# Kernel tuning notes

Measured on AMD Instinct MI355X. Metric: run time of the kernel, lower is better.

## Reference

```python
import jax, jax.numpy as jnp
import numpy as np


def conv1x1(x, W, b):
    # x: [B,C,H,W], W: [O,C] (1x1 conv kernel squeezed), b: [O]
    return jnp.einsum('bchw,oc->bohw', x, W) + b[None, :, None, None]


def setup_inputs() -> dict:
    key = jax.random.key(0)
    ks = jax.random.split(key, 16)
    B, C, H, W = 4, 2048, 32, 32
    HID = 256  # gate_strength_fc hidden width
    s = 1.0 / np.sqrt(C)
    x = jax.random.normal(ks[0], (B, C, H, W), dtype=jnp.float32)
    mask = jax.random.uniform(ks[1], (B, 1, H, W)) > 0.8
    use_entropy_gate = jax.random.randint(ks[2], (B,), 0, 2).astype(bool)
    return {
        'x': x,
        'Wq': jax.random.normal(ks[3], (C, C)) * s,
        'bq': jnp.zeros((C,), jnp.float32),
        'Wk': jax.random.normal(ks[4], (C, C)) * s,
        'bk': jnp.zeros((C,), jnp.float32),
        'Wv': jax.random.normal(ks[5], (C, C)) * s,
        'bv': jnp.zeros((C,), jnp.float32),
        'Wg': jax.random.normal(ks[6], (C, C)) * s,
        'bg': jnp.zeros((C,), jnp.float32),
        'W1': jax.random.normal(ks[7], (HID, C)) * s,
        'b1': jnp.zeros((HID,), jnp.float32),
        'W2': jax.random.normal(ks[8], (1, HID)) * (1.0 / np.sqrt(HID)),
        'b2': jnp.zeros((1,), jnp.float32),
        'mask': mask,
        'use_entropy_gate': use_entropy_gate,
    }


def reference(x, Wq, bq, Wk, bk, Wv, bv, Wg, bg, W1, b1, W2, b2, mask, use_entropy_gate):
    B, C, H, W = x.shape
    HW = H * W
    masked_x = x * mask.astype(x.dtype)
    # 1x1 conv projections, flattened over spatial dims
    q = conv1x1(masked_x, Wq, bq).reshape(B, C, HW).transpose(0, 2, 1)  # [B,HW,C]
    k = conv1x1(masked_x, Wk, bk).reshape(B, C, HW)                     # [B,C,HW]
    v = conv1x1(x, Wv, bv).reshape(B, C, HW)                            # [B,C,HW]
    # attention[b,n,m] = softmax_m(q[b,n,:] . k[b,:,m])
    attn = jax.nn.softmax(jnp.einsum('bnc,bcm->bnm', q, k), axis=-1)    # [B,HW,HW]
    # out = bmm(value, attention^T): out[b,c,m] = sum_n v[b,c,n] * attn[b,m,n]
    out = jnp.einsum('bcn,bmn->bcm', v, attn).reshape(B, C, H, W)
    # gate strength head: 2048 -> 256 -> 1, then sigmoid
    gate_strength = jax.nn.sigmoid(conv1x1(jax.nn.relu(conv1x1(x, W1, b1)), W2, b2))  # [B,1,H,W]
    gate = jax.nn.sigmoid(conv1x1(x, Wg, bg))                                          # [B,C,H,W]
    gated = out * gate * gate_strength
    # per-sample select: gated attention output where flag set, else passthrough x
    return jnp.where(use_entropy_gate[:, None, None, None], gated, x)
```

## Files before the change

kernel.cpp:

```cpp
#include <hip/hip_runtime.h>
#include <cstddef>
#include <cstdint>


typedef unsigned int u32;
typedef unsigned short u16;
typedef __attribute__((ext_vector_type(8))) short bf16x8;
typedef __attribute__((ext_vector_type(4))) float f32x4;

#define B_   4
#define C_   2048
#define HW_  1024
#define HID_ 256
#define KP   384
#define NQK  384
#define NVGH 1088

#define WAITVM(N) asm volatile("s_waitcnt vmcnt(" #N ")" ::: "memory")
__device__ __forceinline__ void barw() {
  asm volatile("" ::: "memory");
  __builtin_amdgcn_s_barrier();
  asm volatile("" ::: "memory");
}

__device__ __forceinline__ float sigmoidf_(float x) {
  return 1.0f / (1.0f + __expf(-x));
}
__device__ __forceinline__ u16 f2bf(float f) {
  u32 u = __float_as_uint(f);
  return (u16)((u + 0x7FFFu + ((u >> 16) & 1u)) >> 16);
}
__device__ __forceinline__ float bf2f(u16 h) {
  return __uint_as_float(((u32)h) << 16);
}
__device__ __forceinline__ void gld16(void* lds, const void* g) {
  __builtin_amdgcn_global_load_lds(
      (const __attribute__((address_space(1))) u32*)g,
      (__attribute__((address_space(3))) u32*)lds, 16, 0, 0);
}

__device__ __forceinline__ void stage128x32s(u16* lds, const u16* g, int ld, int tid) {
#pragma unroll
  for (int t = 0; t < 2; ++t) {
    int s = tid + t * 256;
    int row = s >> 2;
    int oct = ((s & 3) - (row >> 1)) & 3;
    gld16(lds + (size_t)s * 8, g + (size_t)row * ld + oct * 8);
  }
}
template <int NF>
__device__ __forceinline__ void read_frags_s(const u16* lds, int base, int ln, int kq,
                                             bf16x8* f) {
#pragma unroll
  for (int t = 0; t < NF; ++t) {
    int row = base + t * 16 + ln;
    int oct = (kq + (row >> 1)) & 3;
    f[t] = *(const bf16x8*)(lds + (size_t)row * 32 + oct * 8);
  }
}

__device__ __forceinline__ void stage_qk4(u16* L, const u16* Ah, const u16* Al,
                                          const u16* Bh, const u16* Bl, int k0, int tid) {
  stage128x32s(L,         Ah + k0, C_, tid);
  stage128x32s(L + 4096,  Al + k0, C_, tid);
  stage128x32s(L + 8192,  Bh + k0, C_, tid);
  stage128x32s(L + 12288, Bl + k0, C_, tid);
}
__device__ __forceinline__ void stage_ab2(u16* L, const u16* A, const u16* Bp, int k0,
                                          int lda, int ldb, int tid) {
  stage128x32s(L,        A + k0, lda, tid);
  stage128x32s(L + 4096, Bp + k0, ldb, tid);
}
__device__ __forceinline__ void comp_qk(const u16* L, int wm, int wn, int ln, int kq,
                                        f32x4 (&acc)[4][4]) {
  bf16x8 ah[4], al[4], bh[4], bl[4];
  read_frags_s<4>(L, wm, ln, kq, ah);
  read_frags_s<4>(L + 4096, wm, ln, kq, al);
  read_frags_s<4>(L + 8192, wn, ln, kq, bh);
  read_frags_s<4>(L + 12288, wn, ln, kq, bl);
#pragma unroll
  for (int i = 0; i < 4; ++i)
#pragma unroll
    for (int j = 0; j < 4; ++j) {
      acc[i][j] = __builtin_amdgcn_mfma_f32_16x16x32_bf16(ah[i], bh[j], acc[i][j], 0, 0, 0);
      acc[i][j] = __builtin_amdgcn_mfma_f32_16x16x32_bf16(ah[i], bl[j], acc[i][j], 0, 0, 0);
      acc[i][j] = __builtin_amdgcn_mfma_f32_16x16x32_bf16(al[i], bh[j], acc[i][j], 0, 0, 0);
    }
}
__device__ __forceinline__ void comp_ab(const u16* L, int wm, int wn, int ln, int kq,
                                        f32x4 (&acc)[4][4]) {
  bf16x8 af[4], bg_[4];
  read_frags_s<4>(L, wm, ln, kq, af);
  read_frags_s<4>(L + 4096, wn, ln, kq, bg_);
#pragma unroll
  for (int i = 0; i < 4; ++i)
#pragma unroll
    for (int j = 0; j < 4; ++j)
      acc[i][j] = __builtin_amdgcn_mfma_f32_16x16x32_bf16(af[i], bg_[j], acc[i][j], 0, 0, 0);
}

__global__ __launch_bounds__(256)
void scan_mask(const int* __restrict__ mask, int* __restrict__ idx,
               int* __restrict__ rnk, int* __restrict__ cnt)
{
  const int b = blockIdx.x;
  const int t = threadIdx.x;
  __shared__ int base;
  if (t == 0) base = 0;
  __syncthreads();
  int m0 = t * 4;
  int mv[4], local = 0;
#pragma unroll
  for (int i = 0; i < 4; ++i) { mv[i] = mask[b * HW_ + m0 + i] != 0; local += mv[i]; }
  int my = atomicAdd(&base, local);
#pragma unroll
  for (int i = 0; i < 4; ++i) {
    if (mv[i]) {
      int r = my++;
      if (r < KP) { idx[b * KP + r] = m0 + i; rnk[b * HW_ + m0 + i] = r; }
      else rnk[b * HW_ + m0 + i] = -1;
    } else {
      rnk[b * HW_ + m0 + i] = -1;
    }
  }
  __syncthreads();
  if (t == 0) cnt[b] = min(base, KP);
}

__global__ __launch_bounds__(256)
void transpose_fused(const float* __restrict__ x, u16* __restrict__ xhi,
                     u16* __restrict__ xkh, u16* __restrict__ xkl,
                     const int* __restrict__ rnk, const int* __restrict__ useg)
{
  const int b = blockIdx.z;
  if (!useg[b]) return;
  __shared__ float t[32][33];
  const int c0 = blockIdx.y * 32, j0 = blockIdx.x * 32;
  const int tid = threadIdx.x;
  const float* xb = x + ((size_t)b * C_ + c0) * (size_t)HW_ + j0;
  {
    int jj = tid & 31, cs = tid >> 5;
#pragma unroll
    for (int t4 = 0; t4 < 4; ++t4) {
      int c = cs * 4 + t4;
      t[c][jj] = xb[(size_t)c * HW_ + jj];
    }
  }
  __syncthreads();
  int j = tid >> 3, c4 = (tid & 7) * 4;
  float v0 = t[c4 + 0][j], v1 = t[c4 + 1][j], v2 = t[c4 + 2][j], v3 = t[c4 + 3][j];
  ushort4 hv;
  hv.x = f2bf(v0); hv.y = f2bf(v1); hv.z = f2bf(v2); hv.w = f2bf(v3);
  *(ushort4*)(xhi + ((size_t)b * HW_ + j0 + j) * (size_t)C_ + c0 + c4) = hv;
  int r = rnk[b * HW_ + j0 + j];
  if (r >= 0) {
    ushort4 lv;
    lv.x = f2bf(v0 - bf2f(hv.x)); lv.y = f2bf(v1 - bf2f(hv.y));
    lv.z = f2bf(v2 - bf2f(hv.z)); lv.w = f2bf(v3 - bf2f(hv.w));
    size_t o = ((size_t)b * KP + r) * (size_t)C_ + c0 + c4;
    *(ushort4*)(xkh + o) = hv;
    *(ushort4*)(xkl + o) = lv;
  }
}

__global__ __launch_bounds__(256)
void cast_all(const float* __restrict__ Wq, const float* __restrict__ Wk,
              const float* __restrict__ Wv, const float* __restrict__ Wg,
              const float* __restrict__ W1,
              u16* __restrict__ Wqkh, u16* __restrict__ Wqkl, u16* __restrict__ Wvgh)
{
  const int reg = blockIdx.y;
  int i = (blockIdx.x * 256 + threadIdx.x) * 4;
  const float* src; u16* dh; u16* dl = nullptr; int n = C_ * C_;
  if (reg == 0)      { src = Wq; dh = Wqkh;              dl = Wqkl; }
  else if (reg == 1) { src = Wk; dh = Wqkh + C_ * C_;    dl = Wqkl + C_ * C_; }
  else if (reg == 2) { src = Wv; dh = Wvgh; }
  else if (reg == 3) { src = Wg; dh = Wvgh + C_ * C_; }
  else               { src = W1; dh = Wvgh + 2 * C_ * C_; n = HID_ * C_; }
  if (i >= n) return;
  float4 v = *(const float4*)(src + i);
  ushort4 h;
  h.x = f2bf(v.x); h.y = f2bf(v.y); h.z = f2bf(v.z); h.w = f2bf(v.w);
  *(ushort4*)(dh + i) = h;
  if (dl) {
    ushort4 l;
    l.x = f2bf(v.x - bf2f(h.x)); l.y = f2bf(v.y - bf2f(h.y));
    l.z = f2bf(v.z - bf2f(h.z)); l.w = f2bf(v.w - bf2f(h.w));
    *(ushort4*)(dl + i) = l;
  }
}

__global__ __launch_bounds__(256, 2)
void mega2_proj(const u16* __restrict__ Wqkh, const u16* __restrict__ Wqkl,
                const u16* __restrict__ xkh, const u16* __restrict__ xkl,
                const u16* __restrict__ Wvgh, const u16* __restrict__ xhi,
                const float* __restrict__ bq, const float* __restrict__ bk,
                const float* __restrict__ bv, const float* __restrict__ bg,
                const float* __restrict__ b1,
                u16* __restrict__ qTh, u16* __restrict__ qTl,
                u16* __restrict__ kTh, u16* __restrict__ kTl,
                u16* __restrict__ vk2, float* __restrict__ sv,
                u16* __restrict__ gate, float* __restrict__ h,
                const int* __restrict__ rnk,
                const int* __restrict__ cnt, const int* __restrict__ useg)
{
  __shared__ u16 lds0[4 * 4096];
  __shared__ u16 lds1[4 * 4096];
  const int tid = threadIdx.x;
  const int w = tid >> 6, lane = tid & 63, ln = lane & 15, kq = lane >> 4;
  const int bid = blockIdx.x;

  if (bid < NQK) {
    const int b = bid & 3;
    if (!useg[b]) return;
    const int rest = bid >> 2;
    const int row0 = (rest / 3) * 128;
    const int col0 = (rest % 3) * 128;
    const int RC = (cnt[b] + 127) & ~127;
    if (col0 >= RC) return;
    const int wm = (w >> 1) * 64, wn = (w & 1) * 64;
    f32x4 acc[4][4];
#pragma unroll
    for (int i = 0; i < 4; ++i)
#pragma unroll
      for (int j = 0; j < 4; ++j) acc[i][j] = (f32x4){0.f, 0.f, 0.f, 0.f};

    const u16* Ahb = Wqkh + (size_t)row0 * C_;
    const u16* Alb = Wqkl + (size_t)row0 * C_;
    const u16* Bhb = xkh + ((size_t)b * KP + col0) * (size_t)C_;
    const u16* Blb = xkl + ((size_t)b * KP + col0) * (size_t)C_;

    stage_qk4(lds0, Ahb, Alb, Bhb, Blb, 0, tid);
    stage_qk4(lds1, Ahb, Alb, Bhb, Blb, 32, tid);
    u16 *Lc = lds0, *Ln = lds1;
    for (int t = 0; t + 2 < 64; ++t) {
      WAITVM(8); barw();
      comp_qk(Lc, wm, wn, ln, kq, acc);
      barw();
      stage_qk4(Lc, Ahb, Alb, Bhb, Blb, (t + 2) * 32, tid);
      u16* tp = Lc; Lc = Ln; Ln = tp;
    }
    WAITVM(8); barw();
    comp_qk(Lc, wm, wn, ln, kq, acc);
    barw();
    { u16* tp = Lc; Lc = Ln; Ln = tp; }
    WAITVM(0); barw();
    comp_qk(Lc, wm, wn, ln, kq, acc);

    const int half = row0 >= C_;
    const float* bias = half ? bk : bq;
    u16* Oh = half ? kTh : qTh;
    u16* Ol = half ? kTl : qTl;
    const int mbase = row0 - (half ? C_ : 0);
#pragma unroll
    for (int i = 0; i < 4; ++i) {
      int m = mbase + wm + i * 16 + kq * 4;
      float b4[4];
#pragma unroll
      for (int r = 0; r < 4; ++r) b4[r] = bias[m + r];
#pragma unroll
      for (int j = 0; j < 4; ++j) {
        int n = col0 + wn + j * 16 + ln;
        float v0 = acc[i][j][0] + b4[0];
        float v1 = acc[i][j][1] + b4[1];
        float v2 = acc[i][j][2] + b4[2];
        float v3 = acc[i][j][3] + b4[3];
        ushort4 hv, lv;
        hv.x = f2bf(v0); lv.x = f2bf(v0 - bf2f(hv.x));
        hv.y = f2bf(v1); lv.y = f2bf(v1 - bf2f(hv.y));
        hv.z = f2bf(v2); lv.z = f2bf(v2 - bf2f(hv.z));
        hv.w = f2bf(v3); lv.w = f2bf(v3 - bf2f(hv.w));
        size_t o = ((size_t)b * KP + n) * (size_t)C_ + m;
        *(ushort4*)(Oh + o) = hv;
        *(ushort4*)(Ol + o) = lv;
      }
    }
  } else {
    const int bid2 = bid - NQK;
    const int col = bid2 & 7;
    const int b = (bid2 >> 3) & 3;
    const int row0 = (bid2 >> 5) * 128;
    if (!useg[b]) return;
    const int pix0 = col * 128;
    const int wm = (w >> 1) * 64, wn = (w & 1) * 64;
    f32x4 acc[4][4];
#pragma unroll
    for (int i = 0; i < 4; ++i)
#pragma unroll
      for (int j = 0; j < 4; ++j) acc[i][j] = (f32x4){0.f, 0.f, 0.f, 0.f};

    const u16* Ab = Wvgh + (size_t)row0 * C_;
    const u16* Bb = xhi + ((size_t)b * HW_ + pix0) * (size_t)C_;

    stage_ab2(lds0, Ab, Bb, 0, C_, C_, tid);
    stage_ab2(lds1, Ab, Bb, 32, C_, C_, tid);
    u16 *Lc = lds0, *Ln = lds1;
    for (int t = 0; t + 2 < 64; ++t) {
      WAITVM(4); barw();
      comp_ab(Lc, wm, wn, ln, kq, acc);
      barw();
      stage_ab2(Lc, Ab, Bb, (t + 2) * 32, C_, C_, tid);
      u16* tp = Lc; Lc = Ln; Ln = tp;
    }
    WAITVM(4); barw();
    comp_ab(Lc, wm, wn, ln, kq, acc);
    barw();
    { u16* tp = Lc; Lc = Ln; Ln = tp; }
    WAITVM(0); barw();
    comp_ab(Lc, wm, wn, ln, kq, acc);

    const int sect = (row0 >= 2 * C_) ? 2 : (row0 >= C_ ? 1 : 0);
    const float* bias = (sect == 0) ? bv : (sect == 1 ? bg : b1);
    const int sbase = (sect == 0) ? 0 : (sect == 1 ? C_ : 2 * C_);
#pragma unroll
    for (int i = 0; i < 4; ++i) {
      int ml = row0 - sbase + wm + i * 16 + kq * 4;
      float b4[4];
#pragma unroll
      for (int r = 0; r < 4; ++r) b4[r] = bias[ml + r];
      float srow[4] = {0.f, 0.f, 0.f, 0.f};
#pragma unroll
      for (int j = 0; j < 4; ++j) {
        int pp = pix0 + wn + j * 16 + ln;
        int rv = (sect == 0) ? rnk[b * HW_ + pp] : 0;
#pragma unroll
        for (int r = 0; r < 4; ++r) {
          float val = acc[i][j][r] + b4[r];
          if (sect == 0) {
            srow[r] += val;
            if (rv >= 0) vk2[((size_t)b * C_ + ml + r) * (size_t)KP + rv] = f2bf(val);
          } else if (sect == 1) {
            gate[((size_t)b * C_ + ml + r) * (size_t)HW_ + pp] = f2bf(sigmoidf_(val));
          } else {
            h[((size_t)b * HID_ + ml + r) * (size_t)HW_ + pp] = fmaxf(val, 0.f);
          }
        }
      }
      if (sect == 0) {
#pragma unroll
        for (int r = 0; r < 4; ++r) {
          float s = srow[r];
          s += __shfl_down(s, 8);
          s += __shfl_down(s, 4);
          s += __shfl_down(s, 2);
          s += __shfl_down(s, 1);
          if (ln == 0) atomicAdd(&sv[(size_t)b * C_ + ml + r], s);
        }
      }
    }
  }
}

__global__ __launch_bounds__(256, 2)
void logits_splitk(const u16* __restrict__ qTh, const u16* __restrict__ qTl,
                   const u16* __restrict__ kTh, const u16* __restrict__ kTl,
                   float* __restrict__ lk, const int* __restrict__ cnt,
                   const int* __restrict__ useg)
{
  const int b = blockIdx.z >> 3, ks = blockIdx.z & 7;
  if (!useg[b]) return;
  const int RC = (cnt[b] + 127) & ~127;
  const int row0 = blockIdx.y * 128, col0 = blockIdx.x * 128;
  if (row0 >= RC || col0 >= RC) return;
  __shared__ u16 lds0[4 * 4096];
  __shared__ u16 lds1[4 * 4096];
  const int tid = threadIdx.x;
  const int w = tid >> 6, lane = tid & 63, ln = lane & 15, kq = lane >> 4;
  const int wm = (w >> 1) * 64, wn = (w & 1) * 64;
  f32x4 acc[4][4];
#pragma unroll
  for (int i = 0; i < 4; ++i)
#pragma unroll
    for (int j = 0; j < 4; ++j) acc[i][j] = (f32x4){0.f, 0.f, 0.f, 0.f};

  const size_t bs = (size_t)b * KP * (size_t)C_;
  const u16* Ahb = qTh + bs + (size_t)row0 * C_;
  const u16* Alb = qTl + bs + (size_t)row0 * C_;
  const u16* Bhb = kTh + bs + (size_t)col0 * C_;
  const u16* Blb = kTl + bs + (size_t)col0 * C_;
  const int kbeg = ks * 256;

  stage_qk4(lds0, Ahb, Alb, Bhb, Blb, kbeg, tid);
  stage_qk4(lds1, Ahb, Alb, Bhb, Blb, kbeg + 32, tid);
  u16 *Lc = lds0, *Ln = lds1;
  for (int t = 0; t + 2 < 8; ++t) {
    WAITVM(8); barw();
    comp_qk(Lc, wm, wn, ln, kq, acc);
    barw();
    stage_qk4(Lc, Ahb, Alb, Bhb, Blb, kbeg + (t + 2) * 32, tid);
    u16* tp = Lc; Lc = Ln; Ln = tp;
  }
  WAITVM(8); barw();
  comp_qk(Lc, wm, wn, ln, kq, acc);
  barw();
  { u16* tp = Lc; Lc = Ln; Ln = tp; }
  WAITVM(0); barw();
  comp_qk(Lc, wm, wn, ln, kq, acc);

#pragma unroll
  for (int i = 0; i < 4; ++i) {
    int m = row0 + wm + i * 16 + kq * 4;
#pragma unroll
    for (int j = 0; j < 4; ++j) {
      int n = col0 + wn + j * 16 + ln;
#pragma unroll
      for (int r = 0; r < 4; ++r)
        atomicAdd(&lk[((size_t)b * KP + m + r) * (size_t)KP + n], acc[i][j][r]);
    }
  }
}

__global__ __launch_bounds__(256)
void softmax_ind(const float* __restrict__ lk, const int* __restrict__ rnk,
                 const int* __restrict__ cnt, const int* __restrict__ useg,
                 u16* __restrict__ attn_k, float* __restrict__ cm)
{
  const int b = blockIdx.y;
  if (!useg[b]) return;
  const int mo = blockIdx.x;
  const int t = threadIdx.x;
  const int r = rnk[b * HW_ + mo];
  if (r < 0) {
    if (t == 0) cm[b * HW_ + mo] = 1.0f / HW_;
    return;
  }
  const int n = cnt[b];
  const float* row = lk + ((size_t)b * KP + r) * (size_t)KP;
  float v0 = -1e30f, v1 = -1e30f;
  if (t < n) v0 = row[t];
  if (t + 256 < n) v1 = row[t + 256];

  float mx = fmaxf(fmaxf(v0, v1), 0.0f);
#pragma unroll
  for (int off = 32; off > 0; off >>= 1) mx = fmaxf(mx, __shfl_down(mx, off));
  __shared__ float red[8];
  const int wid = t >> 6;
  if ((t & 63) == 0) red[wid] = mx;
  __syncthreads();
  if (t == 0) red[4] = fmaxf(fmaxf(red[0], red[1]), fmaxf(red[2], red[3]));
  __syncthreads();
  mx = red[4];

  float e0 = (t < n) ? __expf(v0 - mx) : 0.f;
  float e1 = (t + 256 < n) ? __expf(v1 - mx) : 0.f;
  float s = e0 + e1;
#pragma unroll
  for (int off = 32; off > 0; off >>= 1) s += __shfl_down(s, off);
  if ((t & 63) == 0) red[wid] = s;
  __syncthreads();
  if (t == 0) red[5] = red[0] + red[1] + red[2] + red[3] + (HW_ - n) * __expf(-mx);
  __syncthreads();
  float inv = 1.0f / red[5];
  float c = __expf(-mx) * inv;
  if (t == 0) cm[b * HW_ + mo] = c;

  u16* arow = attn_k + ((size_t)b * HW_ + mo) * (size_t)KP;
  if (t < n) arow[t] = f2bf(e0 * inv - c);
  if (t + 256 < n) arow[t + 256] = f2bf(e1 * inv - c);
}

__global__ __launch_bounds__(256)
void gate_strength_k(const float* __restrict__ h, const float* __restrict__ W2,
                     const float* __restrict__ b2, float* __restrict__ gs,
                     const int* __restrict__ useg)
{
  const int b = blockIdx.x >> 4;
  if (!useg[b]) return;
  const int tid = threadIdx.x;
  const int jc = (blockIdx.x & 15) * 64;
  const int j = jc + (tid & 63), is = tid >> 6;
  const float* hb = h + (size_t)b * HID_ * HW_;
  float s = 0.f;
  for (int i = is; i < HID_; i += 4) s = fmaf(W2[i], hb[(size_t)i * HW_ + j], s);
  __shared__ float red[4][64];
  red[is][tid & 63] = s;
  __syncthreads();
  if (is == 0) {
    float tot = red[0][tid] + red[1][tid] + red[2][tid] + red[3][tid];
    gs[(size_t)b * HW_ + j] = sigmoidf_(tot + b2[0]);
  }
}

__global__ __launch_bounds__(256, 2)
void out_compact(const u16* __restrict__ vk2, const u16* __restrict__ attn_k,
                 const float* __restrict__ cm, const float* __restrict__ sv,
                 const u16* __restrict__ gate, const float* __restrict__ gs,
                 const float* __restrict__ x, const int* __restrict__ cnt,
                 const int* __restrict__ useg, float* __restrict__ Out)
{
  const int b = blockIdx.z;
  const int tid = threadIdx.x;
  const int row0 = blockIdx.y * 128, col0 = blockIdx.x * 128;
  if (!useg[b]) {
    const float* xb = x + ((size_t)b * C_ + row0) * (size_t)HW_ + col0;
    float* ob = Out + ((size_t)b * C_ + row0) * (size_t)HW_ + col0;
#pragma unroll
    for (int t = 0; t < 16; ++t) {
      int i2 = tid + t * 256;
      int r = i2 >> 5, c4 = (i2 & 31) * 4;
      *(float4*)(ob + (size_t)r * HW_ + c4) = *(const float4*)(xb + (size_t)r * HW_ + c4);
    }
    return;
  }
  __shared__ u16 lds0[2 * 4096];
  __shared__ u16 lds1[2 * 4096];
  const int w = tid >> 6, lane = tid & 63, ln = lane & 15, kq = lane >> 4;
  const int wm = (w >> 1) * 64, wn = (w & 1) * 64;
  f32x4 acc[4][4];
#pragma unroll
  for (int i = 0; i < 4; ++i)
#pragma unroll
    for (int j = 0; j < 4; ++j) acc[i][j] = (f32x4){0.f, 0.f, 0.f, 0.f};

  const int KR = (cnt[b] + 31) & ~31;
  const int NT = KR / 32;
  const u16* Ab = vk2 + ((size_t)b * C_ + row0) * (size_t)KP;
  const u16* Bb = attn_k + ((size_t)b * HW_ + col0) * (size_t)KP;

  stage_ab2(lds0, Ab, Bb, 0, KP, KP, tid);
  if (NT > 1) stage_ab2(lds1, Ab, Bb, 32, KP, KP, tid);
  u16 *Lc = lds0, *Ln = lds1;
  for (int t = 0; t + 2 < NT; ++t) {
    WAITVM(4); barw();
    comp_ab(Lc, wm, wn, ln, kq, acc);
    barw();
    stage_ab2(Lc, Ab, Bb, (t + 2) * 32, KP, KP, tid);
    u16* tp = Lc; Lc = Ln; Ln = tp;
  }
  if (NT > 1) {
    WAITVM(4); barw();
    comp_ab(Lc, wm, wn, ln, kq, acc);
    barw();
    u16* tp = Lc; Lc = Ln; Ln = tp;
  }
  WAITVM(0); barw();
  comp_ab(Lc, wm, wn, ln, kq, acc);

#pragma unroll
  for (int i = 0; i < 4; ++i) {
    int c = row0 + wm + i * 16 + kq * 4;
    float sv4[4];
#pragma unroll
    for (int r = 0; r < 4; ++r) sv4[r] = sv[(size_t)b * C_ + c + r];
#pragma unroll
    for (int j = 0; j < 4; ++j) {
      int m = col0 + wn + j * 16 + ln;
      float cmv = cm[(size_t)b * HW_ + m];
      float gsv = gs[(size_t)b * HW_ + m];
#pragma unroll
      for (int r = 0; r < 4; ++r) {
        size_t off = ((size_t)b * C_ + c + r) * (size_t)HW_ + m;
        float val = acc[i][j][r] + cmv * sv4[r];
        Out[off] = val * bf2f(gate[off]) * gsv;
      }
    }
  }
}

extern "C" void kernel_launch(void* const* d_in, const int* in_sizes, int n_in,
                              void* d_out, int out_size, void* d_ws, size_t ws_size,
                              hipStream_t stream)
{
  (void)in_sizes; (void)n_in; (void)out_size; (void)ws_size;

  const float* x  = (const float*)d_in[0];
  const float* Wq = (const float*)d_in[1];
  const float* bq = (const float*)d_in[2];
  const float* Wk = (const float*)d_in[3];
  const float* bk = (const float*)d_in[4];
  const float* Wv = (const float*)d_in[5];
  const float* bv = (const float*)d_in[6];
  const float* Wg = (const float*)d_in[7];
  const float* bg = (const float*)d_in[8];
  const float* W1 = (const float*)d_in[9];
  const float* b1 = (const float*)d_in[10];
  const float* W2 = (const float*)d_in[11];
  const float* b2 = (const float*)d_in[12];
  const int* mask = (const int*)d_in[13];
  const int* useg = (const int*)d_in[14];
  float* out = (float*)d_out;

  char* p = (char*)d_ws;
  const size_t SZ_T  = (size_t)B_ * HW_ * C_ * sizeof(u16);
  const size_t SZ_W  = (size_t)2 * C_ * C_ * sizeof(u16);
  const size_t SZ_VG = ((size_t)2 * C_ + HID_) * C_ * sizeof(u16);
  const size_t SZ_XK = (size_t)B_ * KP * C_ * sizeof(u16);

  u16* xhi  = (u16*)p; p += SZ_T;
  u16* Wqkh = (u16*)p; p += SZ_W;
  u16* Wqkl = (u16*)p; p += SZ_W;
  u16* Wvgh = (u16*)p; p += SZ_VG;
  u16* xkh  = (u16*)p; p += SZ_XK;
  u16* xkl  = (u16*)p; p += SZ_XK;
  u16* qTh  = (u16*)p; p += SZ_XK;
  u16* qTl  = (u16*)p; p += SZ_XK;
  u16* kTh  = (u16*)p; p += SZ_XK;
  u16* kTl  = (u16*)p; p += SZ_XK;
  u16* gate = (u16*)p; p += SZ_T;
  u16* vk2  = (u16*)p; p += (size_t)B_ * C_ * KP * sizeof(u16);
  float* h  = (float*)p; p += (size_t)B_ * HID_ * HW_ * sizeof(float);
  float* cm = (float*)p; p += (size_t)B_ * HW_ * sizeof(float);
  float* sv = (float*)p; p += (size_t)B_ * C_ * sizeof(float);
  float* gs = (float*)p; p += (size_t)B_ * HW_ * sizeof(float);
  int* idx = (int*)p; p += (size_t)B_ * KP * sizeof(int);
  int* rnk = (int*)p; p += (size_t)B_ * HW_ * sizeof(int);
  int* cnt = (int*)p; p += 64;

  float* lk     = (float*)Wqkh;
  u16*   attn_k = (u16*)((char*)Wqkh + (size_t)B_ * KP * KP * 4);

  dim3 blk(256);

  scan_mask<<<dim3(B_), blk, 0, stream>>>(mask, idx, rnk, cnt);
  hipMemsetAsync(xkh, 0, SZ_XK, stream);
  hipMemsetAsync(xkl, 0, SZ_XK, stream);
  hipMemsetAsync(vk2, 0, (size_t)B_ * C_ * KP * sizeof(u16), stream);
  hipMemsetAsync(sv, 0, (size_t)B_ * C_ * sizeof(float), stream);
  transpose_fused<<<dim3(HW_ / 32, C_ / 32, B_), blk, 0, stream>>>(
      x, xhi, xkh, xkl, rnk, useg);
  cast_all<<<dim3(4096, 5), blk, 0, stream>>>(Wq, Wk, Wv, Wg, W1, Wqkh, Wqkl, Wvgh);

  mega2_proj<<<dim3(NQK + NVGH), blk, 0, stream>>>(
      Wqkh, Wqkl, xkh, xkl, Wvgh, xhi, bq, bk, bv, bg, b1,
      qTh, qTl, kTh, kTl, vk2, sv, gate, h, rnk, cnt, useg);

  hipMemsetAsync(lk, 0, (size_t)B_ * KP * KP * sizeof(float), stream);
  hipMemsetAsync(attn_k, 0, (size_t)B_ * HW_ * KP * sizeof(u16), stream);

  logits_splitk<<<dim3(KP / 128, KP / 128, B_ * 8), blk, 0, stream>>>(
      qTh, qTl, kTh, kTl, lk, cnt, useg);

  softmax_ind<<<dim3(HW_, B_), blk, 0, stream>>>(lk, rnk, cnt, useg, attn_k, cm);

  gate_strength_k<<<dim3(B_ * 16), blk, 0, stream>>>(h, W2, b2, gs, useg);

  out_compact<<<dim3(HW_ / 128, C_ / 128, B_), blk, 0, stream>>>(
      vk2, attn_k, cm, sv, gate, gs, x, cnt, useg, out);
}
```

Baseline: 384.8 us.

## Compute V only on kept pixels and derive V row-sum via matvec

The V projection GEMM now runs only over the compacted kept-pixel columns (xkh), cutting the V section from 8 pixel tiles to at most 2 per row block and shrinking the grid. The row sum of V over all pixels, previously accumulated from the full V GEMM, is now computed algebraically as Wv times the per-channel pixel sum of x plus HW times bias. The pixel sums are gathered in the transpose kernel with atomics, and a new matvec kernel produces sv. This trades a small extra kernel and atomics for removing most of the V GEMM work and the vk2 memset.

```diff
diff --git a/kernel.cpp b/kernel.cpp
--- a/kernel.cpp
+++ b/kernel.cpp
@@ -14,7 +14,7 @@
 #define HID_ 256
 #define KP   384
 #define NQK  384
-#define NVGH 1088
+#define NVGH 704
 
 #define WAITVM(N) asm volatile("s_waitcnt vmcnt(" #N ")" ::: "memory")
 __device__ __forceinline__ void barw() {
@@ -130,7 +130,8 @@
 __global__ __launch_bounds__(256)
 void transpose_fused(const float* __restrict__ x, u16* __restrict__ xhi,
                      u16* __restrict__ xkh, u16* __restrict__ xkl,
-                     const int* __restrict__ rnk, const int* __restrict__ useg)
+                     const int* __restrict__ rnk, const int* __restrict__ useg,
+                     float* __restrict__ sx)
 {
   const int b = blockIdx.z;
   if (!useg[b]) return;
@@ -160,6 +161,12 @@
     size_t o = ((size_t)b * KP + r) * (size_t)C_ + c0 + c4;
     *(ushort4*)(xkh + o) = hv;
     *(ushort4*)(xkl + o) = lv;
+  }
+  if (tid < 32) {
+    float s = 0.f;
+#pragma unroll
+    for (int jj = 0; jj < 32; ++jj) s += t[tid][jj];
+    atomicAdd(&sx[b * C_ + c0 + tid], s);
   }
 }
 
@@ -190,6 +197,49 @@
   }
 }
 
+__global__ __launch_bounds__(256)
+void sv_matvec(const u16* __restrict__ Wvgh, const float* __restrict__ sx,
+               const float* __restrict__ bv, float* __restrict__ sv)
+{
+  __shared__ float sxl[B_ * C_];
+  const int tid = threadIdx.x;
+  for (int i = tid; i < B_ * C_ / 4; i += 256)
+    ((float4*)sxl)[i] = ((const float4*)sx)[i];
+  __syncthreads();
+  const int c = blockIdx.x * 4 + (tid >> 6);
+  const int lane = tid & 63;
+  const u16* wrow = Wvgh + (size_t)c * C_;
+  float a0 = 0.f, a1 = 0.f, a2 = 0.f, a3 = 0.f;
+#pragma unroll
+  for (int it = 0; it < C_ / 512; ++it) {
+    int k0 = it * 512 + lane * 8;
+    bf16x8 wv = *(const bf16x8*)(wrow + k0);
+#pragma unroll
+    for (int u = 0; u < 8; ++u) {
+      float w = bf2f((u16)wv[u]);
+      int k = k0 + u;
+      a0 = fmaf(w, sxl[k], a0);
+      a1 = fmaf(w, sxl[C_ + k], a1);
+      a2 = fmaf(w, sxl[2 * C_ + k], a2);
+      a3 = fmaf(w, sxl[3 * C_ + k], a3);
+    }
+  }
+#pragma unroll
+  for (int off = 32; off > 0; off >>= 1) {
+    a0 += __shfl_down(a0, off);
+    a1 += __shfl_down(a1, off);
+    a2 += __shfl_down(a2, off);
+    a3 += __shfl_down(a3, off);
+  }
+  if (lane == 0) {
+    float bb = (float)HW_ * bv[c];
+    sv[0 * C_ + c] = a0 + bb;
+    sv[1 * C_ + c] = a1 + bb;
+    sv[2 * C_ + c] = a2 + bb;
+    sv[3 * C_ + c] = a3 + bb;
+  }
+}
+
 __global__ __launch_bounds__(256, 2)
 void mega2_proj(const u16* __restrict__ Wqkh, const u16* __restrict__ Wqkl,
                 const u16* __restrict__ xkh, const u16* __restrict__ xkl,
@@ -199,9 +249,7 @@
                 const float* __restrict__ b1,
                 u16* __restrict__ qTh, u16* __restrict__ qTl,
                 u16* __restrict__ kTh, u16* __restrict__ kTl,
-                u16* __restrict__ vk2, float* __restrict__ sv,
-                u16* __restrict__ gate, float* __restrict__ h,
-                const int* __restrict__ rnk,
+                u16* __restrict__ vk2, u16* __restrict__ gate, float* __restrict__ h,
                 const int* __restrict__ cnt, const int* __restrict__ useg)
 {
   __shared__ u16 lds0[4 * 4096];
@@ -277,11 +325,17 @@
     }
   } else {
     const int bid2 = bid - NQK;
-    const int col = bid2 & 7;
-    const int b = (bid2 >> 3) & 3;
-    const int row0 = (bid2 >> 5) * 128;
+    const int b = bid2 / 176;
+    int rr = bid2 % 176;
     if (!useg[b]) return;
-    const int pix0 = col * 128;
+    int sect, row0, pix0;
+    if (rr < 32)       { sect = 0; row0 = (rr >> 1) * 128;            pix0 = (rr & 1) * 128; }
+    else if (rr < 160) { sect = 1; rr -= 32;  row0 = C_ + (rr >> 3) * 128;     pix0 = (rr & 7) * 128; }
+    else               { sect = 2; rr -= 160; row0 = 2 * C_ + (rr >> 3) * 128; pix0 = (rr & 7) * 128; }
+    if (sect == 0) {
+      const int KC = (cnt[b] + 127) & ~127;
+      if (pix0 >= KC) return;
+    }
     const int wm = (w >> 1) * 64, wn = (w & 1) * 64;
     f32x4 acc[4][4];
 #pragma unroll
@@ -290,7 +344,8 @@
       for (int j = 0; j < 4; ++j) acc[i][j] = (f32x4){0.f, 0.f, 0.f, 0.f};
 
     const u16* Ab = Wvgh + (size_t)row0 * C_;
-    const u16* Bb = xhi + ((size_t)b * HW_ + pix0) * (size_t)C_;
+    const u16* Bb = (sect == 0) ? (xkh + ((size_t)b * KP + pix0) * (size_t)C_)
+                                : (xhi + ((size_t)b * HW_ + pix0) * (size_t)C_);
 
     stage_ab2(lds0, Ab, Bb, 0, C_, C_, tid);
     stage_ab2(lds1, Ab, Bb, 32, C_, C_, tid);
@@ -309,7 +364,6 @@
     WAITVM(0); barw();
     comp_ab(Lc, wm, wn, ln, kq, acc);
 
-    const int sect = (row0 >= 2 * C_) ? 2 : (row0 >= C_ ? 1 : 0);
     const float* bias = (sect == 0) ? bv : (sect == 1 ? bg : b1);
     const int sbase = (sect == 0) ? 0 : (sect == 1 ? C_ : 2 * C_);
 #pragma unroll
@@ -318,33 +372,19 @@
       float b4[4];
 #pragma unroll
       for (int r = 0; r < 4; ++r) b4[r] = bias[ml + r];
-      float srow[4] = {0.f, 0.f, 0.f, 0.f};
 #pragma unroll
       for (int j = 0; j < 4; ++j) {
         int pp = pix0 + wn + j * 16 + ln;
-        int rv = (sect == 0) ? rnk[b * HW_ + pp] : 0;
 #pragma unroll
         for (int r = 0; r < 4; ++r) {
           float val = acc[i][j][r] + b4[r];
           if (sect == 0) {
-            srow[r] += val;
-            if (rv >= 0) vk2[((size_t)b * C_ + ml + r) * (size_t)KP + rv] = f2bf(val);
+            vk2[((size_t)b * C_ + ml + r) * (size_t)KP + pp] = f2bf(val);
           } else if (sect == 1) {
             gate[((size_t)b * C_ + ml + r) * (size_t)HW_ + pp] = f2bf(sigmoidf_(val));
           } else {
             h[((size_t)b * HID_ + ml + r) * (size_t)HW_ + pp] = fmaxf(val, 0.f);
           }
-        }
-      }
-      if (sect == 0) {
-#pragma unroll
-        for (int r = 0; r < 4; ++r) {
-          float s = srow[r];
-          s += __shfl_down(s, 8);
-          s += __shfl_down(s, 4);
-          s += __shfl_down(s, 2);
-          s += __shfl_down(s, 1);
-          if (ln == 0) atomicAdd(&sv[(size_t)b * C_ + ml + r], s);
         }
       }
     }
@@ -602,6 +642,7 @@
   float* cm = (float*)p; p += (size_t)B_ * HW_ * sizeof(float);
   float* sv = (float*)p; p += (size_t)B_ * C_ * sizeof(float);
   float* gs = (float*)p; p += (size_t)B_ * HW_ * sizeof(float);
+  float* sx = (float*)p; p += (size_t)B_ * C_ * sizeof(float);
   int* idx = (int*)p; p += (size_t)B_ * KP * sizeof(int);
   int* rnk = (int*)p; p += (size_t)B_ * HW_ * sizeof(int);
   int* cnt = (int*)p; p += 64;
@@ -614,15 +655,15 @@
   scan_mask<<<dim3(B_), blk, 0, stream>>>(mask, idx, rnk, cnt);
   hipMemsetAsync(xkh, 0, SZ_XK, stream);
   hipMemsetAsync(xkl, 0, SZ_XK, stream);
-  hipMemsetAsync(vk2, 0, (size_t)B_ * C_ * KP * sizeof(u16), stream);
-  hipMemsetAsync(sv, 0, (size_t)B_ * C_ * sizeof(float), stream);
+  hipMemsetAsync(sx, 0, (size_t)B_ * C_ * sizeof(float), stream);
   transpose_fused<<<dim3(HW_ / 32, C_ / 32, B_), blk, 0, stream>>>(
-      x, xhi, xkh, xkl, rnk, useg);
+      x, xhi, xkh, xkl, rnk, useg, sx);
   cast_all<<<dim3(4096, 5), blk, 0, stream>>>(Wq, Wk, Wv, Wg, W1, Wqkh, Wqkl, Wvgh);
+  sv_matvec<<<dim3(C_ / 4), blk, 0, stream>>>(Wvgh, sx, bv, sv);
 
   mega2_proj<<<dim3(NQK + NVGH), blk, 0, stream>>>(
       Wqkh, Wqkl, xkh, xkl, Wvgh, xhi, bq, bk, bv, bg, b1,
-      qTh, qTl, kTh, kTl, vk2, sv, gate, h, rnk, cnt, useg);
+      qTh, qTl, kTh, kTl, vk2, gate, h, cnt, useg);
 
   hipMemsetAsync(lk, 0, (size_t)B_ * KP * KP * sizeof(float), stream);
   hipMemsetAsync(attn_k, 0, (size_t)B_ * HW_ * KP * sizeof(u16), stream);
```

Result: faster. 357.0 us (-7.2%).
